# Optimization experiments

Measured on AMD Instinct MI355X. Metric: run time of the kernel, lower is better.

## Reference

```python
import jax, jax.numpy as jnp
import numpy as np
import math

NUM_HEADS = 16
TOPK = 64
EMBED = 1024

def setup_inputs() -> dict:
    key = jax.random.key(0)
    ks = jax.random.split(key, 11)
    b, s, e = 2, 2048, EMBED
    scale = 1.0 / math.sqrt(e)
    inp = {
        'q': jax.random.normal(ks[0], (b, s, e), dtype=jnp.float32),
        'k': jax.random.normal(ks[1], (b, s, e), dtype=jnp.float32),
        'v': jax.random.normal(ks[2], (b, s, e), dtype=jnp.float32),
        'Wq': jax.random.normal(ks[3], (e, e), dtype=jnp.float32) * scale,
        'bq': jnp.zeros((e,), dtype=jnp.float32),
        'Wk': jax.random.normal(ks[4], (e, e), dtype=jnp.float32) * scale,
        'bk': jnp.zeros((e,), dtype=jnp.float32),
        'Wv': jax.random.normal(ks[5], (e, e), dtype=jnp.float32) * scale,
        'bv': jnp.zeros((e,), dtype=jnp.float32),
        'Wo': jax.random.normal(ks[6], (e, e), dtype=jnp.float32) * scale,
        'bo': jnp.zeros((e,), dtype=jnp.float32),
    }
    return inp

def _topk_attention(Q, K, V, topk):
    # Q,K,V: (b, h, s, d)
    d = Q.shape[-1]
    scores = jnp.einsum('bhqd,bhkd->bhqk', Q, K) / jnp.sqrt(jnp.asarray(d, Q.dtype))
    topk_scores, topk_idx = jax.lax.top_k(scores, topk)  # (b,h,s,topk)
    probs = jax.nn.softmax(topk_scores, axis=-1)
    # gather V rows per (b,h): V_bh[idx] -> (s, topk, d); avoids (b,h,s,s,d) expand
    gather = jax.vmap(jax.vmap(lambda Vbh, idx: Vbh[idx]))
    sel = gather(V, topk_idx)  # (b,h,s,topk,d)
    return jnp.einsum('bhqk,bhqkd->bhqd', probs, sel)

def reference(q, k, v, Wq, bq, Wk, bk, Wv, bv, Wo, bo):
    b, s, e = q.shape
    h = NUM_HEADS
    d = e // h
    # NOTE: original torch code reshapes (b, s, e) -> (b, h, s, d) directly (no transpose)
    Q = (q @ Wq.T + bq).reshape(b, h, s, d)
    K = (k @ Wk.T + bk).reshape(b, h, s, d)
    V = (v @ Wv.T + bv).reshape(b, h, s, d)
    attn = _topk_attention(Q, K, V, TOPK)  # (b,h,s,d)
    out = attn.reshape(b, s, e)
    return out @ Wo.T + bo
```

## Files before the change

kernel.cpp:

```cpp
#include <hip/hip_runtime.h>
#include <stdint.h>

using u8  = unsigned char;
using s8  = signed char;
using u16 = unsigned short;
using u32 = unsigned int;
using u64 = unsigned long long;

typedef int   v4i __attribute__((ext_vector_type(4)));
typedef float v4f __attribute__((ext_vector_type(4)));
typedef short v8s __attribute__((ext_vector_type(8)));

__device__ __forceinline__ u16 f2bf(float f){
  u32 u = __builtin_bit_cast(u32, f);
  u32 r = (u + 0x7FFFu + ((u >> 16) & 1u)) >> 16;
  return (u16)r;
}
__device__ __forceinline__ float bf2f(u16 b){
  u32 u = ((u32)b) << 16;
  return __builtin_bit_cast(float, u);
}

__global__ __launch_bounds__(256) void quant_digits(
    const float* __restrict__ in, s8* __restrict__ dig, int n, float scale, float clampv)
{
  int t = blockIdx.x * 256 + threadIdx.x;
  int n8 = n >> 3;
  if (t >= n8) return;
  const float4* inv = (const float4*)in;
  float4 a = inv[2*t], b = inv[2*t+1];
  float xs[8] = {a.x,a.y,a.z,a.w,b.x,b.y,b.z,b.w};
  u64 p0=0,p1=0,p2=0,p3=0;
#pragma unroll
  for (int j=0;j<8;j++){
    float xv = fminf(fmaxf(xs[j], -clampv), clampv);
    int X = (int)rintf(xv * scale);
    int d0 = (int)(s8)(X & 255); X = (X - d0) >> 8;
    int d1 = (int)(s8)(X & 255); X = (X - d1) >> 8;
    int d2 = (int)(s8)(X & 255); X = (X - d2) >> 8;
    int d3 = X;
    p0 |= ((u64)(u8)(s8)d0) << (8*j);
    p1 |= ((u64)(u8)(s8)d1) << (8*j);
    p2 |= ((u64)(u8)(s8)d2) << (8*j);
    p3 |= ((u64)(u8)(s8)d3) << (8*j);
  }
  u64* o = (u64*)dig;
  size_t np8 = (size_t)n8;
  o[t] = p0; o[np8 + t] = p1; o[2*np8 + t] = p2; o[3*np8 + t] = p3;
}

#define MFMA_I8(c, a, b) asm volatile("v_mfma_i32_16x16x64_i8 %0, %1, %2, %0" : "+v"(c) : "v"(a), "v"(b))

__global__ __launch_bounds__(256) void gemm_i8(
    const s8* __restrict__ Ad, const s8* __restrict__ Wd, const float* __restrict__ bias,
    double* __restrict__ Cd, u16* __restrict__ Cb)
{
  __shared__ alignas(16) s8 As[4][64][80];
  __shared__ alignas(16) s8 Bs[4][64][80];
  const int i0 = blockIdx.x * 64, o0 = blockIdx.y * 64;
  const int t = threadIdx.x, w = t >> 6, lane = t & 63;
  const int wr = w >> 1, wc = w & 1, l15 = lane & 15, lg = lane >> 4;
  const int sr = (t >> 2) & 63, sc = (t & 3) << 4;
  const size_t APL = 4194304, WPL = 1048576;

  v4i acc[2][2][4];
#pragma unroll
  for (int tr = 0; tr < 2; ++tr)
#pragma unroll
    for (int tc = 0; tc < 2; ++tc)
#pragma unroll
      for (int c = 0; c < 4; ++c) acc[tr][tc][c] = (v4i){0,0,0,0};

  for (int kt = 0; kt < 16; ++kt){
#pragma unroll
    for (int p = 0; p < 4; ++p){
      int4 av = *(const int4*)(Ad + (size_t)p*APL + (size_t)(i0+sr)*1024 + kt*64 + sc);
      *(int4*)&As[p][sr][sc] = av;
      int4 bv = *(const int4*)(Wd + (size_t)p*WPL + (size_t)(o0+sr)*1024 + kt*64 + sc);
      *(int4*)&Bs[p][sr][sc] = bv;
    }
    __syncthreads();
    v4i af[2][4], bf[2][4];
#pragma unroll
    for (int tr = 0; tr < 2; ++tr)
#pragma unroll
      for (int p = 0; p < 4; ++p){
        af[tr][p] = *(const v4i*)&As[p][wr*32 + tr*16 + l15][lg*16];
        bf[tr][p] = *(const v4i*)&Bs[p][wc*32 + tr*16 + l15][lg*16];
      }
#pragma unroll
    for (int tr = 0; tr < 2; ++tr)
#pragma unroll
      for (int tc = 0; tc < 2; ++tc){
        MFMA_I8(acc[tr][tc][0], af[tr][0], bf[tc][3]);
        MFMA_I8(acc[tr][tc][0], af[tr][1], bf[tc][2]);
        MFMA_I8(acc[tr][tc][0], af[tr][2], bf[tc][1]);
        MFMA_I8(acc[tr][tc][0], af[tr][3], bf[tc][0]);
        MFMA_I8(acc[tr][tc][1], af[tr][1], bf[tc][3]);
        MFMA_I8(acc[tr][tc][1], af[tr][2], bf[tc][2]);
        MFMA_I8(acc[tr][tc][1], af[tr][3], bf[tc][1]);
        MFMA_I8(acc[tr][tc][2], af[tr][2], bf[tc][3]);
        MFMA_I8(acc[tr][tc][2], af[tr][3], bf[tc][2]);
        MFMA_I8(acc[tr][tc][3], af[tr][3], bf[tc][3]);
      }
    __syncthreads();
  }
#pragma unroll
  for (int tr = 0; tr < 2; ++tr)
#pragma unroll
    for (int tc = 0; tc < 2; ++tc){
      const int oc = o0 + wc*32 + tc*16 + l15;
      const double bv = (double)bias[oc];
#pragma unroll
      for (int e = 0; e < 4; ++e){
        double val = (double)acc[tr][tc][0][e]*0x1p-35 + (double)acc[tr][tc][1][e]*0x1p-27
                   + (double)acc[tr][tc][2][e]*0x1p-19 + (double)acc[tr][tc][3][e]*0x1p-11 + bv;
        int orow = i0 + wr*32 + tr*16 + lg*4 + e;
        size_t idx = (size_t)orow*1024 + oc;
        Cd[idx] = val;
        Cb[idx] = f2bf((float)val);
      }
    }
}

template<int ABF16, int OUTBF>
__global__ __launch_bounds__(256) void gemm_bf16k(
    const void* __restrict__ Ap, const float* __restrict__ W, const float* __restrict__ bias,
    void* __restrict__ C)
{
  __shared__ alignas(16) u16 As[64][72];
  __shared__ alignas(16) u16 Bs[64][72];
  const int i0 = blockIdx.x * 64, o0 = blockIdx.y * 64;
  const int t = threadIdx.x, w = t >> 6, lane = t & 63;
  const int wr = w >> 1, wc = w & 1, l15 = lane & 15, lg = lane >> 4;
  const int sr = t >> 2, sc = (t & 3) << 4;

  v4f acc[2][2];
#pragma unroll
  for (int tr = 0; tr < 2; ++tr)
#pragma unroll
    for (int tc = 0; tc < 2; ++tc) acc[tr][tc] = (v4f){0.f,0.f,0.f,0.f};

  for (int kt = 0; kt < 16; ++kt){
    if (ABF16){
      const u16* A = (const u16*)Ap;
      v8s x0 = *(const v8s*)(A + (size_t)(i0+sr)*1024 + kt*64 + sc);
      v8s x1 = *(const v8s*)(A + (size_t)(i0+sr)*1024 + kt*64 + sc + 8);
      *(v8s*)&As[sr][sc] = x0;
      *(v8s*)&As[sr][sc+8] = x1;
    } else {
      const float* A = (const float*)Ap;
      v8s pk0, pk1;
#pragma unroll
      for (int h = 0; h < 2; ++h){
        const float4 y0 = *(const float4*)(A + (size_t)(i0+sr)*1024 + kt*64 + sc + h*8);
        const float4 y1 = *(const float4*)(A + (size_t)(i0+sr)*1024 + kt*64 + sc + h*8 + 4);
        v8s& pk = h ? pk1 : pk0;
        pk[0]=(short)f2bf(y0.x); pk[1]=(short)f2bf(y0.y); pk[2]=(short)f2bf(y0.z); pk[3]=(short)f2bf(y0.w);
        pk[4]=(short)f2bf(y1.x); pk[5]=(short)f2bf(y1.y); pk[6]=(short)f2bf(y1.z); pk[7]=(short)f2bf(y1.w);
      }
      *(v8s*)&As[sr][sc] = pk0;
      *(v8s*)&As[sr][sc+8] = pk1;
    }
    {
      v8s pk0, pk1;
#pragma unroll
      for (int h = 0; h < 2; ++h){
        const float4 y0 = *(const float4*)(W + (size_t)(o0+sr)*1024 + kt*64 + sc + h*8);
        const float4 y1 = *(const float4*)(W + (size_t)(o0+sr)*1024 + kt*64 + sc + h*8 + 4);
        v8s& pk = h ? pk1 : pk0;
        pk[0]=(short)f2bf(y0.x); pk[1]=(short)f2bf(y0.y); pk[2]=(short)f2bf(y0.z); pk[3]=(short)f2bf(y0.w);
        pk[4]=(short)f2bf(y1.x); pk[5]=(short)f2bf(y1.y); pk[6]=(short)f2bf(y1.z); pk[7]=(short)f2bf(y1.w);
      }
      *(v8s*)&Bs[sr][sc] = pk0;
      *(v8s*)&Bs[sr][sc+8] = pk1;
    }
    __syncthreads();
    v8s a[2][2], b[2][2];
#pragma unroll
    for (int tr = 0; tr < 2; ++tr)
#pragma unroll
      for (int ks = 0; ks < 2; ++ks){
        a[tr][ks] = *(const v8s*)&As[wr*32 + tr*16 + l15][ks*32 + lg*8];
        b[tr][ks] = *(const v8s*)&Bs[wc*32 + tr*16 + l15][ks*32 + lg*8];
      }
#pragma unroll
    for (int tr = 0; tr < 2; ++tr)
#pragma unroll
      for (int tc = 0; tc < 2; ++tc){
        acc[tr][tc] = __builtin_amdgcn_mfma_f32_16x16x32_bf16(a[tr][0], b[tc][0], acc[tr][tc], 0, 0, 0);
        acc[tr][tc] = __builtin_amdgcn_mfma_f32_16x16x32_bf16(a[tr][1], b[tc][1], acc[tr][tc], 0, 0, 0);
      }
    __syncthreads();
  }
#pragma unroll
  for (int tr = 0; tr < 2; ++tr)
#pragma unroll
    for (int tc = 0; tc < 2; ++tc){
      const int oc = o0 + wc*32 + tc*16 + l15;
      const float bvv = bias[oc];
#pragma unroll
      for (int e = 0; e < 4; ++e){
        int orow = i0 + wr*32 + tr*16 + lg*4 + e;
        size_t idx = (size_t)orow*1024 + oc;
        if (OUTBF) ((u16*)C)[idx] = f2bf(acc[tr][tc][e] + bvv);
        else       ((float*)C)[idx] = acc[tr][tc][e] + bvv;
      }
    }
}

#define CCAP 184
__global__ __launch_bounds__(512, 4) void attn_topk(
    const u16* __restrict__ Qb, const u16* __restrict__ Kb,
    const double* __restrict__ Qd, const double* __restrict__ Kd,
    const u16* __restrict__ Vb, u16* __restrict__ Ab, u32* __restrict__ flags)
{
  __shared__ u32 candL[64*CCAP];
  __shared__ u32 selpL[16*64];
  __shared__ int cntA[64];

  const int lid = blockIdx.y * 32 + blockIdx.x;
  const int bh  = (lid & 7) * 4 + (lid >> 8);
  const int qb  = (lid >> 3) & 31;
  const size_t base = (size_t)(bh >> 4) * 2097152 + (size_t)(bh & 15) * 131072;
  const int q0 = qb * 64;
  const int tid = threadIdx.x, w = tid >> 6, lane = tid & 63;
  const int l15 = lane & 15, lg = lane >> 4;
  const u64 ltmask = (1ull << lane) - 1ull;

  if (tid < 64) cntA[tid] = 0;
  __syncthreads();

  const v4f vzero = {0.f,0.f,0.f,0.f};
  float nrm0, nrm1, nrm2, nrm3;
  {
    v8s aQ[4][2];
    float T0v[4][4];
#pragma unroll
    for (int g = 0; g < 4; ++g){
      const size_t qoff = base + (size_t)(q0 + g*16 + l15)*64 + lg*8;
      aQ[g][0] = *(const v8s*)(Qb + qoff);
      aQ[g][1] = *(const v8s*)(Qb + qoff + 32);
      float nr = 0.f;
#pragma unroll
      for (int m = 0; m < 8; ++m){
        float x0 = bf2f((u16)aQ[g][0][m]), x1 = bf2f((u16)aQ[g][1][m]);
        nr = fmaf(x0,x0,nr); nr = fmaf(x1,x1,nr);
      }
      nr += __shfl_xor(nr,16);
      nr += __shfl_xor(nr,32);
      if (g == 0) nrm0 = nr; else if (g == 1) nrm1 = nr;
      else if (g == 2) nrm2 = nr; else nrm3 = nr;
#pragma unroll
      for (int e = 0; e < 4; ++e)
        T0v[g][e] = 0.2f * sqrtf(__shfl(nr, lg*4 + e));
    }

    const u16* Kw = Kb + base + (size_t)(w*256 + l15)*64 + lg*8;
    v8s b0 = *(const v8s*)(Kw);
    v8s b1 = *(const v8s*)(Kw + 32);

    auto step = [&](int kt, v8s b0c, v8s b1c){
      const u32 col = (u32)(w*256 + kt*16 + l15);
#pragma unroll
      for (int g = 0; g < 4; ++g){
        v4f s = __builtin_amdgcn_mfma_f32_16x16x32_bf16(aQ[g][0], b0c, vzero, 0,0,0);
        s = __builtin_amdgcn_mfma_f32_16x16x32_bf16(aQ[g][1], b1c, s, 0,0,0);
#pragma unroll
        for (int e = 0; e < 4; ++e){
          float sc = s[e]*0.125f;
          if (sc >= T0v[g][e]){
            int row = g*16 + lg*4 + e;
            int pos = atomicAdd(&cntA[row], 1);
            if (pos < CCAP) candL[row*CCAP + pos] = ((u32)f2bf(sc)<<16) | col;
          }
        }
      }
    };

    for (int kt = 0; kt < 15; ++kt){
      v8s n0 = *(const v8s*)(Kw + (size_t)(kt+1)*1024);
      v8s n1 = *(const v8s*)(Kw + (size_t)(kt+1)*1024 + 32);
      step(kt, b0, b1);
      b0 = n0; b1 = n1;
    }
    step(15, b0, b1);
  }
  __syncthreads();

  for (int pass = 0; pass < 4; ++pass){
    const int R0 = pass*16 + w*2;
    const float nrmP = (pass == 0) ? nrm0 : ((pass == 1) ? nrm1 : ((pass == 2) ? nrm2 : nrm3));
    u32 pk0[2], pk1[2], pk2[2], cstore[2], tv[2];
    bool fail[2];

#pragma unroll
    for (int rr = 0; rr < 2; ++rr){
      const int R = R0 + rr;
      int craw = cntA[R];
      fail[rr] = (craw > CCAP);
      cstore[rr] = (u32)(craw > CCAP ? CCAP : craw);
#pragma unroll
      for (int s = 0; s < 3; ++s){
        u32 idx = (u32)(64*s + lane);
        u32 val = (idx < cstore[rr] && idx < CCAP) ? candL[R*CCAP + idx] : 0u;
        if (s == 0) pk0[rr] = val; else if (s == 1) pk1[rr] = val; else pk2[rr] = val;
      }
      tv[rr] = 0u;
    }

    for (int bit = 14; bit >= 0; --bit){
#pragma unroll
      for (int rr = 0; rr < 2; ++rr){
        u32 tt = tv[rr] | (1u << bit);
        int c = (int)__popcll(__ballot((pk0[rr] >> 16) >= tt))
              + (int)__popcll(__ballot((pk1[rr] >> 16) >= tt))
              + (int)__popcll(__ballot((pk2[rr] >> 16) >= tt));
        if (c >= 64) tv[rr] = tt;
      }
    }

    int na[2], nb[2];
#pragma unroll
    for (int rr = 0; rr < 2; ++rr){
      const int R = R0 + rr;
      const int Rl = R & 15;
      float t64f = bf2f((u16)tv[rr]);
      float T0R = 0.2f * sqrtf(__shfl(nrmP, R & 15));
      float thi = t64f + 0.052f, tlo = t64f - 0.052f;
      int a_ = 0, b_ = 0;
#pragma unroll
      for (int s = 0; s < 3; ++s){
        u32 pkv = (s == 0) ? pk0[rr] : ((s == 1) ? pk1[rr] : pk2[rr]);
        bool act = (u32)(64*s + lane) < cstore[rr];
        float v = bf2f((u16)(pkv >> 16));
        bool aut = act && (v > thi);
        bool ban = act && !aut && (v >= tlo);
        u64 ma = __ballot(aut);
        if (aut){
          int pos = a_ + (int)__popcll(ma & ltmask);
          if (pos < 64) selpL[Rl*64 + pos] = pkv;
        }
        a_ += (int)__popcll(ma);
        u64 mb = __ballot(ban);
        if (ban){
          int pos = b_ + (int)__popcll(mb & ltmask);
          if (pos < 64) candL[R*CCAP + pos] = pkv;
        }
        b_ += (int)__popcll(mb);
      }
      bool fl = fail[rr] || (t64f < T0R + 0.055f) || (t64f >= 3.98f) || (b_ > 64);
      fail[rr] = fl;
      if (lane == 0) flags[bh*2048 + q0 + R] = fl ? 1u : 0u;
      na[rr] = fl ? 64 : (a_ > 64 ? 64 : a_);
      nb[rr] = fl ? 0  : b_;
    }
    asm volatile("s_waitcnt lgkmcnt(0)" ::: "memory");
    __builtin_amdgcn_sched_barrier(0);

    const double* Kdh = Kd + base;
    const double* Qdh = Qd + base + (size_t)q0*64;
    u32 bpk[2];
#pragma unroll
    for (int rr = 0; rr < 2; ++rr)
      bpk[rr] = (lane < nb[rr]) ? candL[(R0+rr)*CCAP + lane] : 0u;
    double ac0[2] = {0,0}, ac1[2] = {0,0};
#pragma unroll 4
    for (int j = 0; j < 32; ++j){
#pragma unroll
      for (int rr = 0; rr < 2; ++rr){
        double2 kv = ((const double2*)(Kdh + (size_t)(bpk[rr] & 0x7FFu)*64))[j];
        double2 qv = ((const double2*)(Qdh + (size_t)(R0+rr)*64))[j];
        ac0[rr] = fma(qv.x, kv.x, ac0[rr]);
        ac1[rr] = fma(qv.y, kv.y, ac1[rr]);
      }
    }
    double mv[2]; int mi[2];
#pragma unroll
    for (int rr = 0; rr < 2; ++rr){
      mv[rr] = (lane < nb[rr]) ? (ac0[rr] + ac1[rr]) : -1.0e300;
      mi[rr] = (lane < nb[rr]) ? (int)(bpk[rr] & 0x7FFu) : 0x7FFFFFFF;
    }
    int maxnb = nb[0] > nb[1] ? nb[0] : nb[1];
    int rank[2] = {0,0};
    for (int j = 0; j < maxnb; ++j){
#pragma unroll
      for (int rr = 0; rr < 2; ++rr){
        double ov = __shfl(mv[rr], j); int oi = __shfl(mi[rr], j);
        rank[rr] += (ov > mv[rr] || (ov == mv[rr] && oi < mi[rr])) ? 1 : 0;
      }
    }
#pragma unroll
    for (int rr = 0; rr < 2; ++rr){
      int need = 64 - na[rr]; if (need > nb[rr]) need = nb[rr];
      if (lane < nb[rr] && rank[rr] < need)
        selpL[((R0+rr) & 15)*64 + na[rr] + rank[rr]] = bpk[rr];
    }
    asm volatile("s_waitcnt lgkmcnt(0)" ::: "memory");
    __builtin_amdgcn_sched_barrier(0);

    u32 sidx[2]; float scv[2], pp[2];
#pragma unroll
    for (int rr = 0; rr < 2; ++rr){
      u32 pr = selpL[((R0+rr) & 15)*64 + lane];
      sidx[rr] = pr & 0x7FFu;
      scv[rr] = __builtin_bit_cast(float, pr & 0xFFFF0000u);
    }
#pragma unroll
    for (int rr = 0; rr < 2; ++rr){
      float mx = scv[rr];
#pragma unroll
      for (int off = 32; off; off >>= 1) mx = fmaxf(mx, __shfl_xor(mx, off));
      float p = expf(scv[rr] - mx);
      float Z = p;
#pragma unroll
      for (int off = 32; off; off >>= 1) Z += __shfl_xor(Z, off);
      pp[rr] = p / Z;
    }
    u64 myp0 = ((u64)__builtin_bit_cast(u32, pp[0]) << 32) | (u64)sidx[0];
    u64 myp1 = ((u64)__builtin_bit_cast(u32, pp[1]) << 32) | (u64)sidx[1];

    const int h = lane >> 5, dl = lane & 31;
    float u0[2] = {0,0}, u1[2] = {0,0};
#pragma unroll 4
    for (int j = 0; j < 64; j += 2){
      u64 pr0 = __shfl(myp0, j + h);
      u64 pr1 = __shfl(myp1, j + h);
#pragma unroll
      for (int rr = 0; rr < 2; ++rr){
        u64 pr = (rr == 0) ? pr0 : pr1;
        float pv = __builtin_bit_cast(float, (u32)(pr >> 32));
        u32 vv = *(const u32*)(Vb + base + (size_t)((u32)pr & 0x7FFu)*64 + 2*dl);
        u0[rr] = fmaf(pv, bf2f((u16)(vv & 0xFFFFu)), u0[rr]);
        u1[rr] = fmaf(pv, bf2f((u16)(vv >> 16)),     u1[rr]);
      }
    }
#pragma unroll
    for (int rr = 0; rr < 2; ++rr){
      u0[rr] += __shfl_xor(u0[rr], 32);
      u1[rr] += __shfl_xor(u1[rr], 32);
    }
    if (lane < 32){
#pragma unroll
      for (int rr = 0; rr < 2; ++rr){
        u32 o = (u32)f2bf(u0[rr]) | ((u32)f2bf(u1[rr]) << 16);
        *(u32*)(Ab + base + (size_t)(q0 + R0 + rr)*64 + 2*dl) = o;
      }
    }
  }
}

__global__ __launch_bounds__(256) void attn_fallback(
    const u32* __restrict__ flags, const double* __restrict__ Qd,
    const double* __restrict__ Kd, const u16* __restrict__ Vb,
    u16* __restrict__ Ab)
{
  __shared__ double ktileL[4][16*64];
  __shared__ double valsL[2048];
  __shared__ double qlds[64];
  __shared__ double selvL[64];
  __shared__ int    seliL[64];
  __shared__ float  ppL[64];
  __shared__ float  ovL[4][64];
  __shared__ double redv[4];
  __shared__ int    redi[4];
  __shared__ double bcv;
  __shared__ int    bci;
  __shared__ u32    mskL;

  const int blk = blockIdx.x;
  const int tid = threadIdx.x, w = tid >> 6, lane = tid & 63;

  if (tid == 0){
    u32 m = 0;
    for (int i = 0; i < 16; ++i) m |= (flags[blk*16 + i] ? 1u : 0u) << i;
    mskL = m;
  }
  __syncthreads();
  const u32 msk = mskL;
  if (msk == 0u) return;

  for (int i = 0; i < 16; ++i){
    if (!((msk >> i) & 1u)) continue;
    const int g = blk*16 + i;
    const int bh = g >> 11, qrow = g & 2047;
    const size_t base = (size_t)(bh >> 4)*2097152 + (size_t)(bh & 15)*131072;
    if (tid < 64) qlds[tid] = Qd[base + (size_t)qrow*64 + tid];
    __syncthreads();

    double* ktw = ktileL[w];
    const int gg = lane >> 4, r = lane & 15;
    for (int t = 0; t < 32; ++t){
      const int k0 = w*512 + t*16;
#pragma unroll
      for (int r2 = 0; r2 < 16; ++r2)
        ktw[r2*64 + ((lane + r2) & 63)] = Kd[base + (size_t)(k0 + r2)*64 + lane];
      double p = 0.0;
#pragma unroll
      for (int dd = 0; dd < 16; ++dd){
        int d = gg*16 + dd;
        p = fma(qlds[d], ktw[r*64 + ((d + r) & 63)], p);
      }
      p += __shfl_xor(p, 16);
      p += __shfl_xor(p, 32);
      if (lane < 16) valsL[k0 + lane] = p * 0.125;
    }
    __syncthreads();

    double myv[8];
#pragma unroll
    for (int m2 = 0; m2 < 8; ++m2) myv[m2] = valsL[tid*8 + m2];

    double pvv = 1.0e300; int pii = -1;
    for (int step = 0; step < 64; ++step){
      double bv = -1.0e300; int bi = 0x7FFFFFFF;
#pragma unroll
      for (int m2 = 0; m2 < 8; ++m2){
        double vv = myv[m2]; int col = tid*8 + m2;
        bool after = (vv < pvv) || (vv == pvv && col > pii);
        bool bet = after && (vv > bv || (vv == bv && col < bi));
        bv = bet ? vv : bv; bi = bet ? col : bi;
      }
#pragma unroll
      for (int off = 32; off; off >>= 1){
        double ov = __shfl_xor(bv, off); int oi = __shfl_xor(bi, off);
        bool tk = (ov > bv) || (ov == bv && oi < bi);
        bv = tk ? ov : bv; bi = tk ? oi : bi;
      }
      if (lane == 0){ redv[w] = bv; redi[w] = bi; }
      __syncthreads();
      if (tid == 0){
        double fv = redv[0]; int fi = redi[0];
#pragma unroll
        for (int x = 1; x < 4; ++x){
          bool tk = (redv[x] > fv) || (redv[x] == fv && redi[x] < fi);
          fv = tk ? redv[x] : fv; fi = tk ? redi[x] : fi;
        }
        bcv = fv; bci = fi; selvL[step] = fv; seliL[step] = fi;
      }
      __syncthreads();
      pvv = bcv; pii = bci;
    }

    if (w == 0){
      float sc = (float)selvL[lane];
      float mx = sc;
#pragma unroll
      for (int off = 32; off; off >>= 1) mx = fmaxf(mx, __shfl_xor(mx, off));
      float p = expf(sc - mx);
      float Z = p;
#pragma unroll
      for (int off = 32; off; off >>= 1) Z += __shfl_xor(Z, off);
      ppL[lane] = p / Z;
    }
    __syncthreads();

    float o = 0.f;
#pragma unroll
    for (int j = 0; j < 16; ++j){
      int jj = w*16 + j;
      o = fmaf(ppL[jj], bf2f(Vb[base + (size_t)seliL[jj]*64 + lane]), o);
    }
    ovL[w][lane] = o;
    __syncthreads();
    if (w == 0){
      float oo = (ovL[0][lane] + ovL[1][lane]) + (ovL[2][lane] + ovL[3][lane]);
      Ab[base + (size_t)qrow*64 + lane] = f2bf(oo);
    }
    __syncthreads();
  }
}

extern "C" void kernel_launch(void* const* d_in, const int* in_sizes, int n_in,
                              void* d_out, int out_size, void* d_ws, size_t ws_size,
                              hipStream_t stream)
{
  (void)in_sizes; (void)n_in; (void)out_size; (void)ws_size;
  const float* q  = (const float*)d_in[0];
  const float* k  = (const float*)d_in[1];
  const float* v  = (const float*)d_in[2];
  const float* Wq = (const float*)d_in[3];
  const float* bq = (const float*)d_in[4];
  const float* Wk = (const float*)d_in[5];
  const float* bk = (const float*)d_in[6];
  const float* Wv = (const float*)d_in[7];
  const float* bv = (const float*)d_in[8];
  const float* Wo = (const float*)d_in[9];
  const float* bo = (const float*)d_in[10];

  char* ws = (char*)d_ws;
  const size_t MB = 1048576;
  double* Qd  = (double*)(ws);
  double* Kd  = (double*)(ws + 32*MB);
  u16*    Qb  = (u16*)  (ws + 64*MB);
  u16*    Kb  = (u16*)  (ws + 72*MB);
  u16*    Abf = (u16*)  (ws + 80*MB);
  s8*     dact= (s8*)   (ws + 88*MB);
  u16*    Vbf = (u16*)  (ws + 88*MB);
  s8*     dw  = (s8*)   (ws + 104*MB);
  u32*    flg = (u32*)  (ws + 104*MB);

  quant_digits<<<2048, 256, 0, stream>>>(q,  dact, 4194304, 134217728.0f, 7.75f);
  quant_digits<<<512,  256, 0, stream>>>(Wq, dw,   1048576, 4294967296.0f, 0.2495f);
  gemm_i8<<<dim3(64, 16), 256, 0, stream>>>(dact, dw, bq, Qd, Qb);
  quant_digits<<<2048, 256, 0, stream>>>(k,  dact, 4194304, 134217728.0f, 7.75f);
  quant_digits<<<512,  256, 0, stream>>>(Wk, dw,   1048576, 4294967296.0f, 0.2495f);
  gemm_i8<<<dim3(64, 16), 256, 0, stream>>>(dact, dw, bk, Kd, Kb);
  gemm_bf16k<0,1><<<dim3(64, 16), 256, 0, stream>>>(v, Wv, bv, Vbf);
  attn_topk<<<dim3(32, 32), 512, 0, stream>>>(Qb, Kb, Qd, Kd, Vbf, Abf, flg);
  attn_fallback<<<4096, 256, 0, stream>>>(flg, Qd, Kd, Vbf, Abf);
  gemm_bf16k<1,0><<<dim3(64, 16), 256, 0, stream>>>(Abf, Wo, bo, d_out);
}
```

Before: 570.4 us.

## Merge quant launches, deepen K prefetch, batch V gathers, coarsen fallback blocks

Merges the activation and weight quantization launches into one kernel that picks its inputs by block index, removing two launches. In attn_topk, the K tile loads are prefetched two steps ahead instead of one, and the V gather loop is restructured to issue four independent loads before the FMAs, exposing more memory-level parallelism. The fallback kernel now builds its flag mask with a wavefront ballot and handles 64 rows per block, so it launches 1024 blocks instead of 4096 and spends less on blocks that exit early. These changes raise register pressure and make each fallback block do more serial work when flags are set.

```diff
diff --git a/kernel.cpp b/kernel.cpp
--- a/kernel.cpp
+++ b/kernel.cpp
@@ -21,10 +21,14 @@
   return __builtin_bit_cast(float, u);
 }
 
-__global__ __launch_bounds__(256) void quant_digits(
-    const float* __restrict__ in, s8* __restrict__ dig, int n, float scale, float clampv)
+__global__ __launch_bounds__(256) void quant_digits2(
+    const float* __restrict__ inA, s8* __restrict__ digA, int nA, float scaleA, float clampA,
+    const float* __restrict__ inW, s8* __restrict__ digW, int nW, float scaleW, float clampW)
 {
-  int t = blockIdx.x * 256 + threadIdx.x;
+  const int bid = blockIdx.x;
+  const float* in; s8* dig; int n; float scale, clampv; int t;
+  if (bid < 2048){ in = inA; dig = digA; n = nA; scale = scaleA; clampv = clampA; t = bid*256 + threadIdx.x; }
+  else           { in = inW; dig = digW; n = nW; scale = scaleW; clampv = clampW; t = (bid-2048)*256 + threadIdx.x; }
   int n8 = n >> 3;
   if (t >= n8) return;
   const float4* inv = (const float4*)in;
@@ -257,8 +261,10 @@
     }
 
     const u16* Kw = Kb + base + (size_t)(w*256 + l15)*64 + lg*8;
-    v8s b0 = *(const v8s*)(Kw);
-    v8s b1 = *(const v8s*)(Kw + 32);
+    v8s b0a = *(const v8s*)(Kw);
+    v8s b1a = *(const v8s*)(Kw + 32);
+    v8s b0b = *(const v8s*)(Kw + 1024);
+    v8s b1b = *(const v8s*)(Kw + 1024 + 32);
 
     auto step = [&](int kt, v8s b0c, v8s b1c){
       const u32 col = (u32)(w*256 + kt*16 + l15);
@@ -278,13 +284,15 @@
       }
     };
 
-    for (int kt = 0; kt < 15; ++kt){
-      v8s n0 = *(const v8s*)(Kw + (size_t)(kt+1)*1024);
-      v8s n1 = *(const v8s*)(Kw + (size_t)(kt+1)*1024 + 32);
-      step(kt, b0, b1);
-      b0 = n0; b1 = n1;
-    }
-    step(15, b0, b1);
+    for (int kt = 0; kt < 14; ++kt){
+      v8s n0 = *(const v8s*)(Kw + (size_t)(kt+2)*1024);
+      v8s n1 = *(const v8s*)(Kw + (size_t)(kt+2)*1024 + 32);
+      step(kt, b0a, b1a);
+      b0a = b0b; b1a = b1b;
+      b0b = n0;  b1b = n1;
+    }
+    step(14, b0a, b1a);
+    step(15, b0b, b1b);
   }
   __syncthreads();
 
@@ -422,17 +430,28 @@
 
     const int h = lane >> 5, dl = lane & 31;
     float u0[2] = {0,0}, u1[2] = {0,0};
-#pragma unroll 4
-    for (int j = 0; j < 64; j += 2){
-      u64 pr0 = __shfl(myp0, j + h);
-      u64 pr1 = __shfl(myp1, j + h);
-#pragma unroll
-      for (int rr = 0; rr < 2; ++rr){
-        u64 pr = (rr == 0) ? pr0 : pr1;
-        float pv = __builtin_bit_cast(float, (u32)(pr >> 32));
-        u32 vv = *(const u32*)(Vb + base + (size_t)((u32)pr & 0x7FFu)*64 + 2*dl);
-        u0[rr] = fmaf(pv, bf2f((u16)(vv & 0xFFFFu)), u0[rr]);
-        u1[rr] = fmaf(pv, bf2f((u16)(vv >> 16)),     u1[rr]);
+#pragma unroll
+    for (int jb = 0; jb < 64; jb += 8){
+      u64 prs0[4], prs1[4];
+#pragma unroll
+      for (int qq = 0; qq < 4; ++qq){
+        prs0[qq] = __shfl(myp0, jb + 2*qq + h);
+        prs1[qq] = __shfl(myp1, jb + 2*qq + h);
+      }
+      u32 vvs0[4], vvs1[4];
+#pragma unroll
+      for (int qq = 0; qq < 4; ++qq){
+        vvs0[qq] = *(const u32*)(Vb + base + (size_t)((u32)prs0[qq] & 0x7FFu)*64 + 2*dl);
+        vvs1[qq] = *(const u32*)(Vb + base + (size_t)((u32)prs1[qq] & 0x7FFu)*64 + 2*dl);
+      }
+#pragma unroll
+      for (int qq = 0; qq < 4; ++qq){
+        float pv0 = __builtin_bit_cast(float, (u32)(prs0[qq] >> 32));
+        u0[0] = fmaf(pv0, bf2f((u16)(vvs0[qq] & 0xFFFFu)), u0[0]);
+        u1[0] = fmaf(pv0, bf2f((u16)(vvs0[qq] >> 16)),     u1[0]);
+        float pv1 = __builtin_bit_cast(float, (u32)(prs1[qq] >> 32));
+        u0[1] = fmaf(pv1, bf2f((u16)(vvs1[qq] & 0xFFFFu)), u0[1]);
+        u1[1] = fmaf(pv1, bf2f((u16)(vvs1[qq] >> 16)),     u1[1]);
       }
     }
 #pragma unroll
@@ -466,23 +485,23 @@
   __shared__ int    redi[4];
   __shared__ double bcv;
   __shared__ int    bci;
-  __shared__ u32    mskL;
+  __shared__ u64    mskL;
 
   const int blk = blockIdx.x;
   const int tid = threadIdx.x, w = tid >> 6, lane = tid & 63;
 
-  if (tid == 0){
-    u32 m = 0;
-    for (int i = 0; i < 16; ++i) m |= (flags[blk*16 + i] ? 1u : 0u) << i;
-    mskL = m;
+  if (tid < 64){
+    u32 f = flags[blk*64 + tid];
+    u64 m = __ballot(f != 0u);
+    if (tid == 0) mskL = m;
   }
   __syncthreads();
-  const u32 msk = mskL;
-  if (msk == 0u) return;
-
-  for (int i = 0; i < 16; ++i){
-    if (!((msk >> i) & 1u)) continue;
-    const int g = blk*16 + i;
+  const u64 msk = mskL;
+  if (msk == 0ull) return;
+
+  for (int i = 0; i < 64; ++i){
+    if (!((msk >> i) & 1ull)) continue;
+    const int g = blk*64 + i;
     const int bh = g >> 11, qrow = g & 2047;
     const size_t base = (size_t)(bh >> 4)*2097152 + (size_t)(bh & 15)*131072;
     if (tid < 64) qlds[tid] = Qd[base + (size_t)qrow*64 + tid];
@@ -600,14 +619,14 @@
   s8*     dw  = (s8*)   (ws + 104*MB);
   u32*    flg = (u32*)  (ws + 104*MB);
 
-  quant_digits<<<2048, 256, 0, stream>>>(q,  dact, 4194304, 134217728.0f, 7.75f);
-  quant_digits<<<512,  256, 0, stream>>>(Wq, dw,   1048576, 4294967296.0f, 0.2495f);
+  quant_digits2<<<2560, 256, 0, stream>>>(q, dact, 4194304, 134217728.0f, 7.75f,
+                                          Wq, dw,  1048576, 4294967296.0f, 0.2495f);
   gemm_i8<<<dim3(64, 16), 256, 0, stream>>>(dact, dw, bq, Qd, Qb);
-  quant_digits<<<2048, 256, 0, stream>>>(k,  dact, 4194304, 134217728.0f, 7.75f);
-  quant_digits<<<512,  256, 0, stream>>>(Wk, dw,   1048576, 4294967296.0f, 0.2495f);
+  quant_digits2<<<2560, 256, 0, stream>>>(k, dact, 4194304, 134217728.0f, 7.75f,
+                                          Wk, dw,  1048576, 4294967296.0f, 0.2495f);
   gemm_i8<<<dim3(64, 16), 256, 0, stream>>>(dact, dw, bk, Kd, Kb);
   gemm_bf16k<0,1><<<dim3(64, 16), 256, 0, stream>>>(v, Wv, bv, Vbf);
   attn_topk<<<dim3(32, 32), 512, 0, stream>>>(Qb, Kb, Qd, Kd, Vbf, Abf, flg);
-  attn_fallback<<<4096, 256, 0, stream>>>(flg, Qd, Kd, Vbf, Abf);
+  attn_fallback<<<1024, 256, 0, stream>>>(flg, Qd, Kd, Vbf, Abf);
   gemm_bf16k<1,0><<<dim3(64, 16), 256, 0, stream>>>(Abf, Wo, bo, d_out);
 }
```

After: 563.4 us. No clear change (-1.2%).
